# Kernel optimization log

Measured on AMD Instinct MI355X. Metric: run time of the kernel, lower is better.

## Reference

```python
import jax, jax.numpy as jnp
import numpy as np
import math

D = 1024
H = 1024
N = 32
T = 1024

def setup_inputs() -> dict:
    key = jax.random.key(0)
    k1, k2, k3, k4 = jax.random.split(key, 4)
    x = jax.random.normal(k1, (N, T, D), dtype=jnp.float32)
    h0 = jax.random.normal(k2, (N, H), dtype=jnp.float32)
    Wx = jax.random.normal(k3, (D, 4 * H), dtype=jnp.float32) / math.sqrt(D)
    Wh = jax.random.normal(k4, (H, 4 * H), dtype=jnp.float32) / math.sqrt(H)
    b = jnp.zeros((4 * H,), dtype=jnp.float32)
    return {"x": x, "h0": h0, "Wx": Wx, "Wh": Wh, "b": b}

def reference(x, h0, Wx, Wh, b):
    # Hoist input projection into one big GEMM: (N,T,D)@(D,4H) -> (N,T,4H)
    xW = jnp.einsum('ntd,dh->nth', x, Wx) + b  # (N, T, 4H)
    Hd = h0.shape[1]

    def step(carry, xw_t):
        prev_h, prev_c = carry
        a = xw_t + prev_h @ Wh  # (N, 4H)
        a_i, a_f, a_o, a_g = jnp.split(a, 4, axis=-1)
        i = jax.nn.sigmoid(a_i)
        f = jax.nn.sigmoid(a_f)
        o = jax.nn.sigmoid(a_o)
        g = jnp.tanh(a_g)
        next_c = f * prev_c + i * g
        next_h = o * jnp.tanh(next_c)
        return (next_h, next_c), next_h

    c0 = jnp.zeros_like(h0)
    xW_t = jnp.swapaxes(xW, 0, 1)  # (T, N, 4H)
    _, hs = jax.lax.scan(step, (h0, c0), xW_t)
    return jnp.swapaxes(hs, 0, 1)  # (N, T, H)
```

## Files before the change

### kernel.cpp

```cpp
#include <hip/hip_runtime.h>
#include <cstdio>
#include <cstdint>

#define TT 1024
#define DD 1024
#define HH 1024
#define NN 32
#define G4 4096

using bf16x8   = __attribute__((ext_vector_type(8))) __bf16;
using f32x4    = __attribute__((ext_vector_type(4))) float;
using uint32x4 = __attribute__((ext_vector_type(4))) unsigned int;

typedef const __attribute__((address_space(1))) void* gas_cp;
typedef __attribute__((address_space(3))) void* las_p;

__device__ __forceinline__ unsigned short f2bf(float f) {
  unsigned int u = __builtin_bit_cast(unsigned int, f);
  u = u + 0x7fffu + ((u >> 16) & 1u);
  return (unsigned short)(u >> 16);
}
__device__ __forceinline__ float bf2f(unsigned short s) {
  unsigned int u = ((unsigned int)s) << 16;
  return __builtin_bit_cast(float, u);
}
__device__ __forceinline__ float sigm(float x) { return 1.f / (1.f + __expf(-x)); }
__device__ __forceinline__ float tanh_f(float x) {
  float a = fabsf(x);
  float e = __expf(-2.f * a);
  float r = (1.f - e) / (1.f + e);
  return x < 0.f ? -r : r;
}

__global__ void cast_bf4(const float4* __restrict__ in, uint2* __restrict__ o, int n4) {
  int i = blockIdx.x * 256 + threadIdx.x;
  if (i < n4) {
    float4 v = in[i];
    uint2 r;
    r.x = (unsigned int)f2bf(v.x) | ((unsigned int)f2bf(v.y) << 16);
    r.y = (unsigned int)f2bf(v.z) | ((unsigned int)f2bf(v.w) << 16);
    o[i] = r;
  }
}

__global__ void transp_cast(const float* __restrict__ in, unsigned short* __restrict__ outT,
                            int R, int C) {
  __shared__ unsigned short t[64][65];
  int nbc = C >> 6;
  int tc = blockIdx.x % nbc, tr = blockIdx.x / nbc;
  int r0 = tr << 6, c0 = tc << 6;
  for (int i = threadIdx.x; i < 4096; i += 256) {
    int r = i >> 6, c = i & 63;
    t[c][r] = f2bf(in[(size_t)(r0 + r) * C + c0 + c]);
  }
  __syncthreads();
  for (int i = threadIdx.x; i < 4096; i += 256) {
    int c = i >> 6, r = i & 63;
    outT[(size_t)(c0 + c) * R + r0 + r] = t[c][r];
  }
}

__global__ void pack_h0(const float* __restrict__ in, unsigned int* __restrict__ o) {
  int i = blockIdx.x * 256 + threadIdx.x;
  o[i] = (unsigned int)f2bf(in[i]);
}

#define BM 128
#define BN 128
#define BK 64

__launch_bounds__(256, 2)
__global__ void gemm_xw(const unsigned short* __restrict__ A,
                        const unsigned short* __restrict__ B,
                        const float* __restrict__ bias,
                        unsigned short* __restrict__ C)
{
  __shared__ alignas(16) unsigned short As[BM * BK];
  __shared__ alignas(16) unsigned short Bs[BN * BK];
  int bid = blockIdx.x;
  int swz = (bid & 7) * 1024 + (bid >> 3);
  int grp = swz >> 8;
  int loc = swz & 255;
  int tm = (grp << 3) + (loc & 7);
  int tn = loc >> 3;
  int tid = threadIdx.x;
  int w = tid >> 6, lane = tid & 63;
  int wr = w >> 1, wc = w & 1;

  f32x4 acc[4][4] = {};

  const size_t rowA0 = (size_t)tm * BM;
  const size_t colB0 = (size_t)tn * BN;

  for (int k0 = 0; k0 < DD; k0 += BK) {
    #pragma unroll
    for (int i = 0; i < 4; ++i) {
      int chunk = w * 4 + i;
      int p = chunk * 1024 + lane * 16;
      int row = p >> 7;
      int bo = p & 127;
      int gb = bo ^ ((row & 7) << 4);
      const char* ga = (const char*)(A + (rowA0 + row) * DD + k0) + gb;
      __builtin_amdgcn_global_load_lds((gas_cp)ga, (las_p)((char*)As + chunk * 1024), 16, 0, 0);
      const char* gB = (const char*)(B + (colB0 + row) * DD + k0) + gb;
      __builtin_amdgcn_global_load_lds((gas_cp)gB, (las_p)((char*)Bs + chunk * 1024), 16, 0, 0);
    }
    __syncthreads();

    #pragma unroll
    for (int ks = 0; ks < 2; ++ks) {
      bf16x8 af[4], bfr[4];
      #pragma unroll
      for (int mi = 0; mi < 4; ++mi) {
        int row = wr * 64 + mi * 16 + (lane & 15);
        int kb = (ks * 32 + ((lane >> 4) << 3)) * 2;
        af[mi] = *(const bf16x8*)((const char*)As + row * 128 + (kb ^ ((row & 7) << 4)));
      }
      #pragma unroll
      for (int ni = 0; ni < 4; ++ni) {
        int row = wc * 64 + ni * 16 + (lane & 15);
        int kb = (ks * 32 + ((lane >> 4) << 3)) * 2;
        bfr[ni] = *(const bf16x8*)((const char*)Bs + row * 128 + (kb ^ ((row & 7) << 4)));
      }
      #pragma unroll
      for (int mi = 0; mi < 4; ++mi)
        #pragma unroll
        for (int ni = 0; ni < 4; ++ni)
          acc[mi][ni] = __builtin_amdgcn_mfma_f32_16x16x32_bf16(af[mi], bfr[ni], acc[mi][ni], 0, 0, 0);
    }
    __syncthreads();
  }

  #pragma unroll
  for (int ni = 0; ni < 4; ++ni) {
    int col = (int)colB0 + wc * 64 + ni * 16 + (lane & 15);
    float bb = bias[col];
    int g = col >> 10, J = col & 1023;
    int jw2 = J >> 5, jc2 = J & 31;
    #pragma unroll
    for (int mi = 0; mi < 4; ++mi) {
      #pragma unroll
      for (int r = 0; r < 4; ++r) {
        size_t row = rowA0 + wr * 64 + mi * 16 + ((lane >> 4) << 2) + r;
        size_t n2 = row >> 10, t2 = row & 1023;
        size_t cl = n2 >> 2, rr = n2 & 3;
        C[((((t2 * 8 + cl) * 32 + jw2) * 4 + rr) * 32 + jc2) * 4 + g] = f2bf(acc[mi][ni][r] + bb);
      }
    }
  }
}

#define LDA0(dst, off) asm volatile("global_load_dwordx2 %0, %1, off offset:" #off " sc0" : "=v"(dst) : "v"(hq))
#define LDA1(dst, off) asm volatile("global_load_dwordx2 %0, %1, off offset:" #off " sc0 sc1" : "=v"(dst) : "v"(hq))
#define LDW(dst, addr, off) asm volatile("global_load_dwordx4 %0, %1, off offset:" #off : "=v"(dst) : "v"(addr))

__launch_bounds__(512, 1)
__global__ void lstm_rec(const unsigned long long* __restrict__ xw,
                         const unsigned short* __restrict__ WhT,
                         unsigned int* __restrict__ hbuf,
                         float* __restrict__ out)
{
  __shared__ float red[2][8][4][128];

  const int bid = blockIdx.x;
  const int cl = bid & 7;
  const int jw = bid >> 3;
  const int j0 = jw * 32;
  const int tid = threadIdx.x;
  const int lane = tid & 63;
  const int kq = tid >> 6;
  const int l15 = lane & 15;
  const int q4 = lane >> 4;

  bf16x8 Bf[8][4];
  #pragma unroll
  for (int tile = 0; tile < 8; ++tile) {
    int cc = tile * 16 + l15;
    int gcol = (cc >> 5) * 1024 + j0 + (cc & 31);
    const unsigned short* wb = WhT + (size_t)gcol * HH + kq * 128 + q4 * 8;
    LDW(Bf[tile][0], wb, 0);
    LDW(Bf[tile][1], wb, 64);
    LDW(Bf[tile][2], wb, 128);
    LDW(Bf[tile][3], wb, 192);
  }
  asm volatile("s_waitcnt vmcnt(0)");

  const bool ld = (l15 < 4);
  const int r4row = lane & 3;
  const int er = tid >> 5, ej = tid & 31;
  float c = 0.f;
  const unsigned long long M64 = 0xFFFF0000FFFF0000ULL;

  unsigned long long u0=0,u1=0,u2=0,u3=0,u4=0,u5=0,u6=0,u7=0,
                     u8=0,u9=0,u10=0,u11=0,u12=0,u13=0,u14=0,u15=0;

  unsigned long long xq = 0;
  if (tid < 128) xq = xw[(((size_t)0 * 8 + cl) * 32 + jw) * 128 + tid];

  #pragma unroll 1
  for (int t = 0; t < TT; ++t) {
    const int par = t & 1;
    const unsigned int* hc = hbuf + (size_t)par * 32768 + cl * 4096;
    unsigned int* hn = hbuf + (size_t)(par ^ 1) * 32768 + cl * 4096;

    const unsigned long long pat =
        ((unsigned long long)(unsigned)t << 16) | ((unsigned long long)(unsigned)t << 48);
    if (ld) {
      const unsigned long long* hq =
          (const unsigned long long*)(hc + r4row * 1024 + kq * 128 + q4 * 8);
      int rc = 0;
      for (;;) {
        if (!(rc & 1)) {
          LDA0(u0,0);   LDA0(u1,8);   LDA0(u2,16);  LDA0(u3,24);
          LDA0(u4,128); LDA0(u5,136); LDA0(u6,144); LDA0(u7,152);
          LDA0(u8,256); LDA0(u9,264); LDA0(u10,272);LDA0(u11,280);
          LDA0(u12,384);LDA0(u13,392);LDA0(u14,400);LDA0(u15,408);
        } else {
          LDA1(u0,0);   LDA1(u1,8);   LDA1(u2,16);  LDA1(u3,24);
          LDA1(u4,128); LDA1(u5,136); LDA1(u6,144); LDA1(u7,152);
          LDA1(u8,256); LDA1(u9,264); LDA1(u10,272);LDA1(u11,280);
          LDA1(u12,384);LDA1(u13,392);LDA1(u14,400);LDA1(u15,408);
        }
        asm volatile("s_waitcnt vmcnt(0)");
        __builtin_amdgcn_sched_barrier(0);
        unsigned long long bad =
            ((u0 & M64) ^ pat)  | ((u1 & M64) ^ pat)  | ((u2 & M64) ^ pat)  | ((u3 & M64) ^ pat)  |
            ((u4 & M64) ^ pat)  | ((u5 & M64) ^ pat)  | ((u6 & M64) ^ pat)  | ((u7 & M64) ^ pat)  |
            ((u8 & M64) ^ pat)  | ((u9 & M64) ^ pat)  | ((u10 & M64) ^ pat) | ((u11 & M64) ^ pat) |
            ((u12 & M64) ^ pat) | ((u13 & M64) ^ pat) | ((u14 & M64) ^ pat) | ((u15 & M64) ^ pat);
        if (!__any(bad != 0)) break;
        __builtin_amdgcn_s_sleep(1);
        ++rc;
      }
    }

    unsigned long long xq_n = 0;
    if (tid < 128) {
      int tp = (t + 1 < TT) ? t + 1 : 0;
      xq_n = xw[(((size_t)tp * 8 + cl) * 32 + jw) * 128 + tid];
    }

    f32x4 acc[8] = {};
    {
      uint32x4 wv;
      #define KSTEP(ks, a0, a1, a2, a3)                                              \
        wv[0] = __builtin_amdgcn_perm((unsigned)((a0) >> 32), (unsigned)(a0), 0x05040100u); \
        wv[1] = __builtin_amdgcn_perm((unsigned)((a1) >> 32), (unsigned)(a1), 0x05040100u); \
        wv[2] = __builtin_amdgcn_perm((unsigned)((a2) >> 32), (unsigned)(a2), 0x05040100u); \
        wv[3] = __builtin_amdgcn_perm((unsigned)((a3) >> 32), (unsigned)(a3), 0x05040100u); \
        { bf16x8 av = __builtin_bit_cast(bf16x8, wv);                                \
          _Pragma("unroll")                                                          \
          for (int tile = 0; tile < 8; ++tile)                                       \
            acc[tile] = __builtin_amdgcn_mfma_f32_16x16x32_bf16(av, Bf[tile][ks], acc[tile], 0, 0, 0); }
      KSTEP(0, u0, u1, u2, u3)
      KSTEP(1, u4, u5, u6, u7)
      KSTEP(2, u8, u9, u10, u11)
      KSTEP(3, u12, u13, u14, u15)
      #undef KSTEP
    }

    if (q4 == 0) {
      #pragma unroll
      for (int tile = 0; tile < 8; ++tile)
        #pragma unroll
        for (int rg = 0; rg < 4; ++rg)
          red[par][kq][rg][tile * 16 + l15] = acc[tile][rg];
    }
    __syncthreads();

    if (tid < 128) {
      float s0 = 0.f, s1 = 0.f, s2 = 0.f, s3 = 0.f;
      #pragma unroll
      for (int k2 = 0; k2 < 8; ++k2) {
        s0 += red[par][k2][er][ej];
        s1 += red[par][k2][er][32 + ej];
        s2 += red[par][k2][er][64 + ej];
        s3 += red[par][k2][er][96 + ej];
      }
      float ai  = s0 + bf2f((unsigned short)xq);
      float af_ = s1 + bf2f((unsigned short)(xq >> 16));
      float ao  = s2 + bf2f((unsigned short)(xq >> 32));
      float ag  = s3 + bf2f((unsigned short)(xq >> 48));
      float ig = sigm(ai), fg = sigm(af_), og = sigm(ao);
      float gg = tanh_f(ag);
      c = fg * c + ig * gg;
      float hv = og * tanh_f(c);

      unsigned int hp = (unsigned int)f2bf(hv) | ((unsigned int)(t + 1) << 16);
      __hip_atomic_store(hn + er * 1024 + j0 + ej, hp,
                         __ATOMIC_RELAXED, __HIP_MEMORY_SCOPE_AGENT);
      out[((size_t)(cl * 4 + er) * TT + t) * HH + j0 + ej] = hv;
    }
    xq = xq_n;
  }
}

extern "C" void kernel_launch(void* const* d_in, const int* in_sizes, int n_in,
                              void* d_out, int out_size, void* d_ws, size_t ws_size,
                              hipStream_t stream) {
  (void)in_sizes; (void)n_in; (void)out_size;
  const float* x  = (const float*)d_in[0];
  const float* h0 = (const float*)d_in[1];
  const float* Wx = (const float*)d_in[2];
  const float* Wh = (const float*)d_in[3];
  const float* b  = (const float*)d_in[4];
  float* out = (float*)d_out;

  char* ws = (char*)d_ws;
  size_t o_xw  = 0;
  size_t o_xbf = o_xw  + (size_t)32768 * 4096 * 2;
  size_t o_wxT = o_xbf + (size_t)32768 * 1024 * 2;
  size_t o_whT = o_wxT + (size_t)4096 * 1024 * 2;
  size_t o_hb  = o_whT + (size_t)4096 * 1024 * 2;
  size_t need  = o_hb  + (size_t)2 * 32768 * 4;
  if (ws_size < need) {
    fprintf(stderr, "kernel_launch: ws_size %zu < needed %zu\n", ws_size, need);
    return;
  }
  unsigned short* xw  = (unsigned short*)(ws + o_xw);
  unsigned short* xbf = (unsigned short*)(ws + o_xbf);
  unsigned short* wxT = (unsigned short*)(ws + o_wxT);
  unsigned short* whT = (unsigned short*)(ws + o_whT);
  unsigned int*   hb  = (unsigned int*)(ws + o_hb);

  hipMemsetAsync(hb, 0xFF, (size_t)2 * 32768 * 4, stream);
  pack_h0<<<128, 256, 0, stream>>>(h0, hb);
  cast_bf4<<<32768, 256, 0, stream>>>((const float4*)x, (uint2*)xbf, 33554432 / 4);
  transp_cast<<<1024, 256, 0, stream>>>(Wx, wxT, 1024, 4096);
  transp_cast<<<1024, 256, 0, stream>>>(Wh, whT, 1024, 4096);
  gemm_xw<<<8192, 256, 0, stream>>>(xbf, wxT, b, xw);

  void* args[] = { (void*)&xw, (void*)&whT, (void*)&hb, (void*)&out };
  hipLaunchCooperativeKernel(lstm_rec, dim3(256), dim3(512), args, 0, stream);
}
```

Measured before the change: 4.490 ms.

## Duplicate hidden-state buffer for polling and keep Wh fragments in AGPRs

Adds a second hidden-state buffer written with a plain volatile store alongside the atomic store. The polling loop reads mostly from this copy with sc0 loads and only falls back to the sc1 path on the original buffer every fourth retry. Wh weight fragments are now loaded straight into accumulation registers, and the MFMA chain is written as inline assembly with explicit nops, which aims to free VGPRs and tighten the per-step matmul. The risks are hazard-timing correctness from the hand-placed nops, extra store traffic per step, and stale reads delaying convergence of the poll.

```diff
diff --git a/kernel.cpp b/kernel.cpp
--- a/kernel.cpp
+++ b/kernel.cpp
@@ -60,9 +60,12 @@
   }
 }
 
-__global__ void pack_h0(const float* __restrict__ in, unsigned int* __restrict__ o) {
+__global__ void pack_h0(const float* __restrict__ in, unsigned int* __restrict__ o1,
+                        unsigned int* __restrict__ o2) {
   int i = blockIdx.x * 256 + threadIdx.x;
-  o[i] = (unsigned int)f2bf(in[i]);
+  unsigned int v = (unsigned int)f2bf(in[i]);
+  o1[i] = v;
+  o2[i] = v;
 }
 
 #define BM 128
@@ -150,14 +153,44 @@
   }
 }
 
-#define LDA0(dst, off) asm volatile("global_load_dwordx2 %0, %1, off offset:" #off " sc0" : "=v"(dst) : "v"(hq))
-#define LDA1(dst, off) asm volatile("global_load_dwordx2 %0, %1, off offset:" #off " sc0 sc1" : "=v"(dst) : "v"(hq))
-#define LDW(dst, addr, off) asm volatile("global_load_dwordx4 %0, %1, off offset:" #off : "=v"(dst) : "v"(addr))
+#define LDA0(dst, ptr, off) asm volatile("global_load_dwordx2 %0, %1, off offset:" #off " sc0" : "=v"(dst) : "v"(ptr))
+#define LDA1(dst, ptr, off) asm volatile("global_load_dwordx2 %0, %1, off offset:" #off " sc0 sc1" : "=v"(dst) : "v"(ptr))
+#define ALD(dst, addr, off) asm volatile("global_load_dwordx4 %0, %1, off offset:" #off : "=a"(dst) : "v"(addr))
+
+#define POLL16(M, P) \
+  M(u0,P,0);   M(u1,P,8);   M(u2,P,16);  M(u3,P,24);  \
+  M(u4,P,128); M(u5,P,136); M(u6,P,144); M(u7,P,152); \
+  M(u8,P,256); M(u9,P,264); M(u10,P,272);M(u11,P,280);\
+  M(u12,P,384);M(u13,P,392);M(u14,P,400);M(u15,P,408)
+
+#define UNPACK(avv, a0, a1, a2, a3) { uint32x4 wv_;                                     \
+  wv_[0] = __builtin_amdgcn_perm((unsigned)((a0) >> 32), (unsigned)(a0), 0x05040100u);  \
+  wv_[1] = __builtin_amdgcn_perm((unsigned)((a1) >> 32), (unsigned)(a1), 0x05040100u);  \
+  wv_[2] = __builtin_amdgcn_perm((unsigned)((a2) >> 32), (unsigned)(a2), 0x05040100u);  \
+  wv_[3] = __builtin_amdgcn_perm((unsigned)((a3) >> 32), (unsigned)(a3), 0x05040100u);  \
+  avv = __builtin_bit_cast(bf16x8, wv_); }
+
+#define MFMA8(tail, av, B0,B1,B2,B3,B4,B5,B6,B7)                      \
+  asm volatile("s_nop 2\n\t"                                          \
+    "v_mfma_f32_16x16x32_bf16 %0, %8, %9, %0\n\t"                     \
+    "v_mfma_f32_16x16x32_bf16 %1, %8, %10, %1\n\t"                    \
+    "v_mfma_f32_16x16x32_bf16 %2, %8, %11, %2\n\t"                    \
+    "v_mfma_f32_16x16x32_bf16 %3, %8, %12, %3\n\t"                    \
+    "v_mfma_f32_16x16x32_bf16 %4, %8, %13, %4\n\t"                    \
+    "v_mfma_f32_16x16x32_bf16 %5, %8, %14, %5\n\t"                    \
+    "v_mfma_f32_16x16x32_bf16 %6, %8, %15, %6\n\t"                    \
+    "v_mfma_f32_16x16x32_bf16 %7, %8, %16, %7\n\t"                    \
+    tail                                                              \
+    : "+v"(acc[0]), "+v"(acc[1]), "+v"(acc[2]), "+v"(acc[3]),         \
+      "+v"(acc[4]), "+v"(acc[5]), "+v"(acc[6]), "+v"(acc[7])          \
+    : "v"(av), "a"(B0), "a"(B1), "a"(B2), "a"(B3),                    \
+      "a"(B4), "a"(B5), "a"(B6), "a"(B7))
 
 __launch_bounds__(512, 1)
 __global__ void lstm_rec(const unsigned long long* __restrict__ xw,
                          const unsigned short* __restrict__ WhT,
                          unsigned int* __restrict__ hbuf,
+                         unsigned int* __restrict__ hbuf2,
                          float* __restrict__ out)
 {
   __shared__ float red[2][8][4][128];
@@ -178,10 +211,10 @@
     int cc = tile * 16 + l15;
     int gcol = (cc >> 5) * 1024 + j0 + (cc & 31);
     const unsigned short* wb = WhT + (size_t)gcol * HH + kq * 128 + q4 * 8;
-    LDW(Bf[tile][0], wb, 0);
-    LDW(Bf[tile][1], wb, 64);
-    LDW(Bf[tile][2], wb, 128);
-    LDW(Bf[tile][3], wb, 192);
+    ALD(Bf[tile][0], wb, 0);
+    ALD(Bf[tile][1], wb, 64);
+    ALD(Bf[tile][2], wb, 128);
+    ALD(Bf[tile][3], wb, 192);
   }
   asm volatile("s_waitcnt vmcnt(0)");
 
@@ -200,27 +233,21 @@
   #pragma unroll 1
   for (int t = 0; t < TT; ++t) {
     const int par = t & 1;
-    const unsigned int* hc = hbuf + (size_t)par * 32768 + cl * 4096;
-    unsigned int* hn = hbuf + (size_t)(par ^ 1) * 32768 + cl * 4096;
+    const unsigned int* hcA = hbuf  + (size_t)par * 32768 + cl * 4096;
+    const unsigned int* hc2 = hbuf2 + (size_t)par * 32768 + cl * 4096;
+    unsigned int* hnA = hbuf  + (size_t)(par ^ 1) * 32768 + cl * 4096;
+    unsigned int* hn2 = hbuf2 + (size_t)(par ^ 1) * 32768 + cl * 4096;
 
     const unsigned long long pat =
         ((unsigned long long)(unsigned)t << 16) | ((unsigned long long)(unsigned)t << 48);
     if (ld) {
-      const unsigned long long* hq =
-          (const unsigned long long*)(hc + r4row * 1024 + kq * 128 + q4 * 8);
+      const size_t idx = (size_t)r4row * 1024 + kq * 128 + q4 * 8;
+      const unsigned long long* hq2 = (const unsigned long long*)(hc2 + idx);
+      const unsigned long long* hqA = (const unsigned long long*)(hcA + idx);
       int rc = 0;
       for (;;) {
-        if (!(rc & 1)) {
-          LDA0(u0,0);   LDA0(u1,8);   LDA0(u2,16);  LDA0(u3,24);
-          LDA0(u4,128); LDA0(u5,136); LDA0(u6,144); LDA0(u7,152);
-          LDA0(u8,256); LDA0(u9,264); LDA0(u10,272);LDA0(u11,280);
-          LDA0(u12,384);LDA0(u13,392);LDA0(u14,400);LDA0(u15,408);
-        } else {
-          LDA1(u0,0);   LDA1(u1,8);   LDA1(u2,16);  LDA1(u3,24);
-          LDA1(u4,128); LDA1(u5,136); LDA1(u6,144); LDA1(u7,152);
-          LDA1(u8,256); LDA1(u9,264); LDA1(u10,272);LDA1(u11,280);
-          LDA1(u12,384);LDA1(u13,392);LDA1(u14,400);LDA1(u15,408);
-        }
+        if ((rc & 3) != 3) { POLL16(LDA0, hq2); }
+        else               { POLL16(LDA1, hqA); }
         asm volatile("s_waitcnt vmcnt(0)");
         __builtin_amdgcn_sched_barrier(0);
         unsigned long long bad =
@@ -240,24 +267,17 @@
       xq_n = xw[(((size_t)tp * 8 + cl) * 32 + jw) * 128 + tid];
     }
 
+    bf16x8 av0, av1, av2, av3;
+    UNPACK(av0, u0,  u1,  u2,  u3)
+    UNPACK(av1, u4,  u5,  u6,  u7)
+    UNPACK(av2, u8,  u9,  u10, u11)
+    UNPACK(av3, u12, u13, u14, u15)
     f32x4 acc[8] = {};
-    {
-      uint32x4 wv;
-      #define KSTEP(ks, a0, a1, a2, a3)                                              \
-        wv[0] = __builtin_amdgcn_perm((unsigned)((a0) >> 32), (unsigned)(a0), 0x05040100u); \
-        wv[1] = __builtin_amdgcn_perm((unsigned)((a1) >> 32), (unsigned)(a1), 0x05040100u); \
-        wv[2] = __builtin_amdgcn_perm((unsigned)((a2) >> 32), (unsigned)(a2), 0x05040100u); \
-        wv[3] = __builtin_amdgcn_perm((unsigned)((a3) >> 32), (unsigned)(a3), 0x05040100u); \
-        { bf16x8 av = __builtin_bit_cast(bf16x8, wv);                                \
-          _Pragma("unroll")                                                          \
-          for (int tile = 0; tile < 8; ++tile)                                       \
-            acc[tile] = __builtin_amdgcn_mfma_f32_16x16x32_bf16(av, Bf[tile][ks], acc[tile], 0, 0, 0); }
-      KSTEP(0, u0, u1, u2, u3)
-      KSTEP(1, u4, u5, u6, u7)
-      KSTEP(2, u8, u9, u10, u11)
-      KSTEP(3, u12, u13, u14, u15)
-      #undef KSTEP
-    }
+    MFMA8("s_nop 4", av0, Bf[0][0],Bf[1][0],Bf[2][0],Bf[3][0],Bf[4][0],Bf[5][0],Bf[6][0],Bf[7][0]);
+    MFMA8("s_nop 4", av1, Bf[0][1],Bf[1][1],Bf[2][1],Bf[3][1],Bf[4][1],Bf[5][1],Bf[6][1],Bf[7][1]);
+    MFMA8("s_nop 4", av2, Bf[0][2],Bf[1][2],Bf[2][2],Bf[3][2],Bf[4][2],Bf[5][2],Bf[6][2],Bf[7][2]);
+    MFMA8("s_nop 7\n\ts_nop 7\n\ts_nop 7", av3,
+          Bf[0][3],Bf[1][3],Bf[2][3],Bf[3][3],Bf[4][3],Bf[5][3],Bf[6][3],Bf[7][3]);
 
     if (q4 == 0) {
       #pragma unroll
@@ -287,7 +307,9 @@
       float hv = og * tanh_f(c);
 
       unsigned int hp = (unsigned int)f2bf(hv) | ((unsigned int)(t + 1) << 16);
-      __hip_atomic_store(hn + er * 1024 + j0 + ej, hp,
+      const size_t ho = (size_t)er * 1024 + j0 + ej;
+      ((volatile unsigned int*)hn2)[ho] = hp;
+      __hip_atomic_store(hnA + ho, hp,
                          __ATOMIC_RELAXED, __HIP_MEMORY_SCOPE_AGENT);
       out[((size_t)(cl * 4 + er) * TT + t) * HH + j0 + ej] = hv;
     }
@@ -312,7 +334,8 @@
   size_t o_wxT = o_xbf + (size_t)32768 * 1024 * 2;
   size_t o_whT = o_wxT + (size_t)4096 * 1024 * 2;
   size_t o_hb  = o_whT + (size_t)4096 * 1024 * 2;
-  size_t need  = o_hb  + (size_t)2 * 32768 * 4;
+  size_t o_hb2 = o_hb  + (size_t)2 * 32768 * 4;
+  size_t need  = o_hb2 + (size_t)2 * 32768 * 4;
   if (ws_size < need) {
     fprintf(stderr, "kernel_launch: ws_size %zu < needed %zu\n", ws_size, need);
     return;
@@ -322,14 +345,16 @@
   unsigned short* wxT = (unsigned short*)(ws + o_wxT);
   unsigned short* whT = (unsigned short*)(ws + o_whT);
   unsigned int*   hb  = (unsigned int*)(ws + o_hb);
+  unsigned int*   hb2 = (unsigned int*)(ws + o_hb2);
 
   hipMemsetAsync(hb, 0xFF, (size_t)2 * 32768 * 4, stream);
-  pack_h0<<<128, 256, 0, stream>>>(h0, hb);
+  hipMemsetAsync(hb2, 0xFF, (size_t)2 * 32768 * 4, stream);
+  pack_h0<<<128, 256, 0, stream>>>(h0, hb, hb2);
   cast_bf4<<<32768, 256, 0, stream>>>((const float4*)x, (uint2*)xbf, 33554432 / 4);
   transp_cast<<<1024, 256, 0, stream>>>(Wx, wxT, 1024, 4096);
   transp_cast<<<1024, 256, 0, stream>>>(Wh, whT, 1024, 4096);
   gemm_xw<<<8192, 256, 0, stream>>>(xbf, wxT, b, xw);
 
-  void* args[] = { (void*)&xw, (void*)&whT, (void*)&hb, (void*)&out };
+  void* args[] = { (void*)&xw, (void*)&whT, (void*)&hb, (void*)&hb2, (void*)&out };
   hipLaunchCooperativeKernel(lstm_rec, dim3(256), dim3(512), args, 0, stream);
 }
```

New measurement: 6.516 ms. 45.1% more time.

## Replace per-step block barrier with LDS flag handoff and relax poll coherence

Applied to the files above, without the earlier changes.

Replaces the per-timestep __syncthreads between the MFMA partial-sum writes and the gate reduction with per-wave sequence flags in LDS. Each wave publishes its flag with a release store, and only the consumer waves spin on all eight flags with acquire loads. Producer waves can therefore start polling for the next timestep's h without waiting for the reduction, taking the block-wide barrier off the serial recurrence path. The h-polling loop now issues the stronger sc0 sc1 loads only on every fourth retry instead of every other one, which lowers the cost of each poll but may take longer to see fresh data. The safety of reusing the double-buffered reduction array now depends on the inter-block h handshake rather than on a barrier.

```diff
diff --git a/kernel.cpp b/kernel.cpp
--- a/kernel.cpp
+++ b/kernel.cpp
@@ -150,9 +150,21 @@
   }
 }
 
-#define LDA0(dst, off) asm volatile("global_load_dwordx2 %0, %1, off offset:" #off " sc0" : "=v"(dst) : "v"(hq))
-#define LDA1(dst, off) asm volatile("global_load_dwordx2 %0, %1, off offset:" #off " sc0 sc1" : "=v"(dst) : "v"(hq))
+#define LDA0(dst, ptr, off) asm volatile("global_load_dwordx2 %0, %1, off offset:" #off " sc0" : "=v"(dst) : "v"(ptr))
+#define LDA1(dst, ptr, off) asm volatile("global_load_dwordx2 %0, %1, off offset:" #off " sc0 sc1" : "=v"(dst) : "v"(ptr))
 #define LDW(dst, addr, off) asm volatile("global_load_dwordx4 %0, %1, off offset:" #off : "=v"(dst) : "v"(addr))
+
+#define POLL16(M, P) \
+  M(u0,P,0);   M(u1,P,8);   M(u2,P,16);  M(u3,P,24);  \
+  M(u4,P,128); M(u5,P,136); M(u6,P,144); M(u7,P,152); \
+  M(u8,P,256); M(u9,P,264); M(u10,P,272);M(u11,P,280);\
+  M(u12,P,384);M(u13,P,392);M(u14,P,400);M(u15,P,408)
+
+#define CHECK16(bad) \
+  bad = ((u0 & M64) ^ pat)  | ((u1 & M64) ^ pat)  | ((u2 & M64) ^ pat)  | ((u3 & M64) ^ pat)  | \
+        ((u4 & M64) ^ pat)  | ((u5 & M64) ^ pat)  | ((u6 & M64) ^ pat)  | ((u7 & M64) ^ pat)  | \
+        ((u8 & M64) ^ pat)  | ((u9 & M64) ^ pat)  | ((u10 & M64) ^ pat) | ((u11 & M64) ^ pat) | \
+        ((u12 & M64) ^ pat) | ((u13 & M64) ^ pat) | ((u14 & M64) ^ pat) | ((u15 & M64) ^ pat)
 
 __launch_bounds__(512, 1)
 __global__ void lstm_rec(const unsigned long long* __restrict__ xw,
@@ -161,6 +173,7 @@
                          float* __restrict__ out)
 {
   __shared__ float red[2][8][4][128];
+  __shared__ unsigned int seqw[8];
 
   const int bid = blockIdx.x;
   const int cl = bid & 7;
@@ -171,6 +184,8 @@
   const int kq = tid >> 6;
   const int l15 = lane & 15;
   const int q4 = lane >> 4;
+
+  if (tid < 8) seqw[tid] = 0;
 
   bf16x8 Bf[8][4];
   #pragma unroll
@@ -184,6 +199,7 @@
     LDW(Bf[tile][3], wb, 192);
   }
   asm volatile("s_waitcnt vmcnt(0)");
+  __syncthreads();
 
   const bool ld = (l15 < 4);
   const int r4row = lane & 3;
@@ -207,27 +223,15 @@
         ((unsigned long long)(unsigned)t << 16) | ((unsigned long long)(unsigned)t << 48);
     if (ld) {
       const unsigned long long* hq =
-          (const unsigned long long*)(hc + r4row * 1024 + kq * 128 + q4 * 8);
+          (const unsigned long long*)(hc + (size_t)r4row * 1024 + kq * 128 + q4 * 8);
       int rc = 0;
       for (;;) {
-        if (!(rc & 1)) {
-          LDA0(u0,0);   LDA0(u1,8);   LDA0(u2,16);  LDA0(u3,24);
-          LDA0(u4,128); LDA0(u5,136); LDA0(u6,144); LDA0(u7,152);
-          LDA0(u8,256); LDA0(u9,264); LDA0(u10,272);LDA0(u11,280);
-          LDA0(u12,384);LDA0(u13,392);LDA0(u14,400);LDA0(u15,408);
-        } else {
-          LDA1(u0,0);   LDA1(u1,8);   LDA1(u2,16);  LDA1(u3,24);
-          LDA1(u4,128); LDA1(u5,136); LDA1(u6,144); LDA1(u7,152);
-          LDA1(u8,256); LDA1(u9,264); LDA1(u10,272);LDA1(u11,280);
-          LDA1(u12,384);LDA1(u13,392);LDA1(u14,400);LDA1(u15,408);
-        }
+        if ((rc & 3) != 3) { POLL16(LDA0, hq); }
+        else               { POLL16(LDA1, hq); }
         asm volatile("s_waitcnt vmcnt(0)");
         __builtin_amdgcn_sched_barrier(0);
-        unsigned long long bad =
-            ((u0 & M64) ^ pat)  | ((u1 & M64) ^ pat)  | ((u2 & M64) ^ pat)  | ((u3 & M64) ^ pat)  |
-            ((u4 & M64) ^ pat)  | ((u5 & M64) ^ pat)  | ((u6 & M64) ^ pat)  | ((u7 & M64) ^ pat)  |
-            ((u8 & M64) ^ pat)  | ((u9 & M64) ^ pat)  | ((u10 & M64) ^ pat) | ((u11 & M64) ^ pat) |
-            ((u12 & M64) ^ pat) | ((u13 & M64) ^ pat) | ((u14 & M64) ^ pat) | ((u15 & M64) ^ pat);
+        unsigned long long bad;
+        CHECK16(bad);
         if (!__any(bad != 0)) break;
         __builtin_amdgcn_s_sleep(1);
         ++rc;
@@ -266,9 +270,17 @@
         for (int rg = 0; rg < 4; ++rg)
           red[par][kq][rg][tile * 16 + l15] = acc[tile][rg];
     }
-    __syncthreads();
+    if (lane == 0)
+      __hip_atomic_store(&seqw[kq], (unsigned)(t + 1),
+                         __ATOMIC_RELEASE, __HIP_MEMORY_SCOPE_WORKGROUP);
 
     if (tid < 128) {
+      const unsigned tgt = (unsigned)(t + 1);
+      for (;;) {
+        unsigned v = __hip_atomic_load(&seqw[lane & 7],
+                                       __ATOMIC_ACQUIRE, __HIP_MEMORY_SCOPE_WORKGROUP);
+        if (__all(v >= tgt)) break;
+      }
       float s0 = 0.f, s1 = 0.f, s2 = 0.f, s3 = 0.f;
       #pragma unroll
       for (int k2 = 0; k2 < 8; ++k2) {
@@ -287,7 +299,7 @@
       float hv = og * tanh_f(c);
 
       unsigned int hp = (unsigned int)f2bf(hv) | ((unsigned int)(t + 1) << 16);
-      __hip_atomic_store(hn + er * 1024 + j0 + ej, hp,
+      __hip_atomic_store(hn + (size_t)er * 1024 + j0 + ej, hp,
                          __ATOMIC_RELAXED, __HIP_MEMORY_SCOPE_AGENT);
       out[((size_t)(cl * 4 + er) * TT + t) * HH + j0 + ej] = hv;
     }
```

After: 6.463 ms. 1.44x slower.
